# Optimization experiments

Measured on AMD Instinct MI355X. Metric: run time of the kernel, lower is better.

The kernel has to match this reference:

```python
import jax, jax.numpy as jnp
import numpy as np

K = 16  # top-k, matches init kwarg k


def _topk_weighted_mean(conn, parent, k):
    """conn: [n, p] weights, parent: [p, d] -> [n, d].
    Faithful to original: argsort()[-k:] top-k, softmax over selected weights,
    then weighted sum of gathered parent rows."""
    idx = jnp.argsort(conn, axis=-1)[:, -k:]                      # [n, k]
    w = jax.nn.softmax(jnp.take_along_axis(conn, idx, axis=-1), axis=-1)  # [n, k]
    return jnp.einsum('nk,nkd->nd', w, parent[idx])               # gather + small matmul


def setup_inputs() -> dict:
    key = jax.random.key(0)
    k_ids, k_c1, k_c2, k_c3, k_root = jax.random.split(key, 5)
    objNum, clusterNums, embedDim = 200000, (1024, 256, 64), 64
    batch = 8192
    return {
        'ids': jax.random.randint(k_ids, (batch,), 0, objNum, dtype=jnp.int64)
               if jax.config.jax_enable_x64 else jax.random.randint(k_ids, (batch,), 0, objNum, dtype=jnp.int32),
        'conn1': jax.random.normal(k_c1, (objNum, clusterNums[0]), jnp.float32),
        'conn2': jax.random.normal(k_c2, (clusterNums[0], clusterNums[1]), jnp.float32),
        'conn3': jax.random.normal(k_c3, (clusterNums[1], clusterNums[2]), jnp.float32),
        'rootMatrix': jax.random.normal(k_root, (clusterNums[2], embedDim), jnp.float32),
    }


def reference(ids, conn1, conn2, conn3, rootMatrix):
    # getEmbedByLevel(2): combine rootMatrix rows -> level-2 cluster embeddings
    e2 = _topk_weighted_mean(conn3, rootMatrix, K)   # [256, d]
    # getEmbedByLevel(1): combine level-2 embeddings -> level-1 cluster embeddings
    e1 = _topk_weighted_mean(conn2, e2, K)           # [1024, d]
    # getEmbed(ids): combine level-1 embeddings per requested leaf object
    return _topk_weighted_mean(conn1[ids], e1, K)    # [B, d]
```

## Files before the change

kernel.cpp:

```cpp
#include <hip/hip_runtime.h>
#include <stdint.h>
#include <math.h>

#define WAVE 64
#define TOPK 16

__device__ __forceinline__ uint32_t f2s(float f) {
    uint32_t u = __float_as_uint(f);
    return u ^ (uint32_t)(((int32_t)u >> 31) | 0x80000000);
}
__device__ __forceinline__ float s2f(uint32_t s) {
    uint32_t u = (s & 0x80000000u) ? (s ^ 0x80000000u) : ~s;
    return __uint_as_float(u);
}
__device__ __forceinline__ uint32_t umax32(uint32_t a, uint32_t b) { return a > b ? a : b; }

__device__ __forceinline__ uint32_t wave_max64(uint32_t m, int xaddr) {
    uint32_t r;
    r = (uint32_t)__builtin_amdgcn_update_dpp((int)m, (int)m, 0x121, 0xF, 0xF, false);
    m = umax32(m, r);
    r = (uint32_t)__builtin_amdgcn_update_dpp((int)m, (int)m, 0x122, 0xF, 0xF, false);
    m = umax32(m, r);
    r = (uint32_t)__builtin_amdgcn_update_dpp((int)m, (int)m, 0x124, 0xF, 0xF, false);
    m = umax32(m, r);
    r = (uint32_t)__builtin_amdgcn_update_dpp((int)m, (int)m, 0x128, 0xF, 0xF, false);
    m = umax32(m, r);
    r = (uint32_t)__builtin_amdgcn_ds_swizzle((int)m, 0x401F);
    m = umax32(m, r);
    r = (uint32_t)__builtin_amdgcn_ds_bpermute(xaddr, (int)m);
    m = umax32(m, r);
    return m;
}

template <int P>
__global__ void topk_wm_kernel(const float* __restrict__ conn,
                               const int* __restrict__ rowsel,
                               const float* __restrict__ parent,
                               float* __restrict__ out,
                               int n) {
    const int lane = threadIdx.x & (WAVE - 1);
    const int row = blockIdx.x * (blockDim.x >> 6) + (threadIdx.x >> 6);
    if (row >= n) return;

    const long src_row = rowsel ? (long)rowsel[row] : (long)row;
    const float* __restrict__ crow = conn + src_row * (long)P;

    constexpr int VPL = P / WAVE;
    uint32_t v[VPL];

    if constexpr (VPL >= 4) {
#pragma unroll
        for (int c = 0; c < VPL / 4; ++c) {
            float4 f4 = *reinterpret_cast<const float4*>(crow + c * (WAVE * 4) + lane * 4);
            v[c * 4 + 0] = f2s(f4.x);
            v[c * 4 + 1] = f2s(f4.y);
            v[c * 4 + 2] = f2s(f4.z);
            v[c * 4 + 3] = f2s(f4.w);
        }
    } else {
        v[0] = f2s(crow[lane]);
    }

    const int xaddr = (lane ^ 32) << 2;

    uint32_t topv[TOPK];
    int topi[TOPK];

#pragma unroll
    for (int t = 0; t < TOPK; ++t) {
        uint32_t m = v[0];
        int li = 0;
#pragma unroll
        for (int j = 1; j < VPL; ++j) {
            bool c = v[j] > m;
            m = c ? v[j] : m;
            li = c ? j : li;
        }
        const uint32_t m0 = m;
        m = wave_max64(m, xaddr);

        unsigned long long ball = __ballot(m0 == m);
        const int srcl = 63 - __builtin_clzll(ball);
        const int lis = __builtin_amdgcn_readlane(li, srcl);

        topv[t] = m;
        if constexpr (VPL >= 4) {
            topi[t] = (lis >> 2) * (WAVE * 4) + srcl * 4 + (lis & 3);
        } else {
            topi[t] = srcl;
        }

        const bool won = (lane == srcl);
#pragma unroll
        for (int j = 0; j < VPL; ++j) {
            if (won && j == lis) v[j] = 0u;
        }
    }

    const float mx = s2f(topv[0]);
    float w[TOPK];
    float ssum = 0.f;
#pragma unroll
    for (int t = 0; t < TOPK; ++t) {
        w[t] = __expf(s2f(topv[t]) - mx);
        ssum += w[t];
    }
    const float inv = 1.0f / ssum;

    float acc = 0.f;
#pragma unroll
    for (int t = 0; t < TOPK; ++t) {
        acc = fmaf(w[t], parent[topi[t] * 64 + lane], acc);
    }
    out[(long)row * 64 + lane] = acc * inv;
}

extern "C" void kernel_launch(void* const* d_in, const int* in_sizes, int n_in,
                              void* d_out, int out_size, void* d_ws, size_t ws_size,
                              hipStream_t stream) {
    const int* ids = (const int*)d_in[0];
    const float* conn1 = (const float*)d_in[1];
    const float* conn2 = (const float*)d_in[2];
    const float* conn3 = (const float*)d_in[3];
    const float* root = (const float*)d_in[4];
    float* out = (float*)d_out;

    const int batch = in_sizes[0];
    const int n1 = 1024, n2 = 256;

    float* e2 = (float*)d_ws;
    float* e1 = e2 + (size_t)n2 * 64;

    dim3 blk(256);

    topk_wm_kernel<64><<<dim3(n2 / 4), blk, 0, stream>>>(conn3, nullptr, root, e2, n2);
    topk_wm_kernel<256><<<dim3(n1 / 4), blk, 0, stream>>>(conn2, nullptr, e2, e1, n1);
    topk_wm_kernel<1024><<<dim3(batch / 4), blk, 0, stream>>>(conn1, ids, e1, out, batch);
}
```

Measured before the change: 36.30 us.

## Pack index into low key bits and pre-sort per-lane values for top-k selection

Each per-lane value is turned into a sortable key with its column index packed into the low bits, and the lane's values are bitonic-sorted in registers. Each top-k step then needs only a wave max of the lane head plus a register shift, with no ballot or readlane of the source lane. The wave reduction uses row_bcast DPP followed by readlane 63 instead of swizzle and bpermute. When the 16th and 17th keys tie in their truncated high bits, the kernel falls back to a full-precision selection pass, and the softmax reloads the exact selected values from memory. This adds in-register sort work per lane and a rarely-taken fallback branch.

```diff
diff --git a/kernel.cpp b/kernel.cpp
--- a/kernel.cpp
+++ b/kernel.cpp
@@ -7,29 +7,31 @@
 
 __device__ __forceinline__ uint32_t f2s(float f) {
     uint32_t u = __float_as_uint(f);
-    return u ^ (uint32_t)(((int32_t)u >> 31) | 0x80000000);
-}
-__device__ __forceinline__ float s2f(uint32_t s) {
-    uint32_t u = (s & 0x80000000u) ? (s ^ 0x80000000u) : ~s;
-    return __uint_as_float(u);
+    return u ^ (uint32_t)(((int32_t)u >> 31) | 0x80000000u);
 }
 __device__ __forceinline__ uint32_t umax32(uint32_t a, uint32_t b) { return a > b ? a : b; }
+__device__ __forceinline__ uint32_t umin32(uint32_t a, uint32_t b) { return a < b ? a : b; }
 
-__device__ __forceinline__ uint32_t wave_max64(uint32_t m, int xaddr) {
-    uint32_t r;
-    r = (uint32_t)__builtin_amdgcn_update_dpp((int)m, (int)m, 0x121, 0xF, 0xF, false);
-    m = umax32(m, r);
-    r = (uint32_t)__builtin_amdgcn_update_dpp((int)m, (int)m, 0x122, 0xF, 0xF, false);
-    m = umax32(m, r);
-    r = (uint32_t)__builtin_amdgcn_update_dpp((int)m, (int)m, 0x124, 0xF, 0xF, false);
-    m = umax32(m, r);
-    r = (uint32_t)__builtin_amdgcn_update_dpp((int)m, (int)m, 0x128, 0xF, 0xF, false);
-    m = umax32(m, r);
-    r = (uint32_t)__builtin_amdgcn_ds_swizzle((int)m, 0x401F);
-    m = umax32(m, r);
-    r = (uint32_t)__builtin_amdgcn_ds_bpermute(xaddr, (int)m);
-    m = umax32(m, r);
-    return m;
+template <int CTRL, int RMASK>
+__device__ __forceinline__ uint32_t dppmax(uint32_t m) {
+    uint32_t r = (uint32_t)__builtin_amdgcn_update_dpp((int)m, (int)m, CTRL, RMASK, 0xF, false);
+    return umax32(m, r);
+}
+
+__device__ __forceinline__ uint32_t wave_umax(uint32_t m) {
+    m = dppmax<0x121, 0xF>(m);
+    m = dppmax<0x122, 0xF>(m);
+    m = dppmax<0x124, 0xF>(m);
+    m = dppmax<0x128, 0xF>(m);
+    m = dppmax<0x142, 0xA>(m);
+    m = dppmax<0x143, 0xC>(m);
+    return (uint32_t)__builtin_amdgcn_readlane((int)m, 63);
+}
+
+template <int VPL>
+__device__ __forceinline__ uint32_t gpos(int j, int lane) {
+    if constexpr (VPL == 1) return (uint32_t)lane;
+    else return (uint32_t)((j >> 2) * (WAVE * 4) + lane * 4 + (j & 3));
 }
 
 template <int P>
@@ -38,6 +40,8 @@
                                const float* __restrict__ parent,
                                float* __restrict__ out,
                                int n) {
+    constexpr int VPL = P / WAVE;
+    constexpr uint32_t IMASK = (uint32_t)(P - 1);
     const int lane = threadIdx.x & (WAVE - 1);
     const int row = blockIdx.x * (blockDim.x >> 6) + (threadIdx.x >> 6);
     if (row >= n) return;
@@ -45,74 +49,107 @@
     const long src_row = rowsel ? (long)rowsel[row] : (long)row;
     const float* __restrict__ crow = conn + src_row * (long)P;
 
-    constexpr int VPL = P / WAVE;
-    uint32_t v[VPL];
-
-    if constexpr (VPL >= 4) {
+    uint32_t k[VPL];
+    if constexpr (VPL == 1) {
+        k[0] = (f2s(crow[lane]) & ~IMASK) | (uint32_t)lane;
+    } else {
 #pragma unroll
         for (int c = 0; c < VPL / 4; ++c) {
             float4 f4 = *reinterpret_cast<const float4*>(crow + c * (WAVE * 4) + lane * 4);
-            v[c * 4 + 0] = f2s(f4.x);
-            v[c * 4 + 1] = f2s(f4.y);
-            v[c * 4 + 2] = f2s(f4.z);
-            v[c * 4 + 3] = f2s(f4.w);
+            const uint32_t b = (uint32_t)(c * (WAVE * 4) + lane * 4);
+            k[c * 4 + 0] = (f2s(f4.x) & ~IMASK) | (b + 0u);
+            k[c * 4 + 1] = (f2s(f4.y) & ~IMASK) | (b + 1u);
+            k[c * 4 + 2] = (f2s(f4.z) & ~IMASK) | (b + 2u);
+            k[c * 4 + 3] = (f2s(f4.w) & ~IMASK) | (b + 3u);
         }
-    } else {
-        v[0] = f2s(crow[lane]);
-    }
-
-    const int xaddr = (lane ^ 32) << 2;
-
-    uint32_t topv[TOPK];
-    int topi[TOPK];
-
 #pragma unroll
-    for (int t = 0; t < TOPK; ++t) {
-        uint32_t m = v[0];
-        int li = 0;
+        for (int size = 2; size <= VPL; size <<= 1) {
 #pragma unroll
-        for (int j = 1; j < VPL; ++j) {
-            bool c = v[j] > m;
-            m = c ? v[j] : m;
-            li = c ? j : li;
-        }
-        const uint32_t m0 = m;
-        m = wave_max64(m, xaddr);
-
-        unsigned long long ball = __ballot(m0 == m);
-        const int srcl = 63 - __builtin_clzll(ball);
-        const int lis = __builtin_amdgcn_readlane(li, srcl);
-
-        topv[t] = m;
-        if constexpr (VPL >= 4) {
-            topi[t] = (lis >> 2) * (WAVE * 4) + srcl * 4 + (lis & 3);
-        } else {
-            topi[t] = srcl;
-        }
-
-        const bool won = (lane == srcl);
+            for (int stride = size >> 1; stride > 0; stride >>= 1) {
 #pragma unroll
-        for (int j = 0; j < VPL; ++j) {
-            if (won && j == lis) v[j] = 0u;
+                for (int i = 0; i < VPL; ++i) {
+                    const int j = i ^ stride;
+                    if (j > i) {
+                        const uint32_t a = k[i], b2 = k[j];
+                        const uint32_t hi = umax32(a, b2), lo = umin32(a, b2);
+                        if ((i & size) == 0) { k[i] = hi; k[j] = lo; }
+                        else                 { k[i] = lo; k[j] = hi; }
+                    }
+                }
+            }
         }
     }
 
-    const float mx = s2f(topv[0]);
-    float w[TOPK];
-    float ssum = 0.f;
+    uint32_t idx[TOPK];
+    uint32_t q16 = 0;
 #pragma unroll
     for (int t = 0; t < TOPK; ++t) {
-        w[t] = __expf(s2f(topv[t]) - mx);
-        ssum += w[t];
+        const uint32_t K = wave_umax(k[0]);
+        idx[t] = K & IMASK;
+        if (t == TOPK - 1) q16 = K & ~IMASK;
+        const bool won = (k[0] == K);
+#pragma unroll
+        for (int j = 0; j < VPL - 1; ++j) k[j] = won ? k[j + 1] : k[j];
+        k[VPL - 1] = won ? 0u : k[VPL - 1];
     }
-    const float inv = 1.0f / ssum;
+    const uint32_t k17 = wave_umax(k[0]);
 
-    float acc = 0.f;
+    if ((k17 & ~IMASK) == q16) {
+        uint32_t v[VPL];
+        if constexpr (VPL == 1) {
+            v[0] = f2s(crow[lane]);
+        } else {
+#pragma unroll
+            for (int c = 0; c < VPL / 4; ++c) {
+                float4 f4 = *reinterpret_cast<const float4*>(crow + c * (WAVE * 4) + lane * 4);
+                v[c * 4 + 0] = f2s(f4.x);
+                v[c * 4 + 1] = f2s(f4.y);
+                v[c * 4 + 2] = f2s(f4.z);
+                v[c * 4 + 3] = f2s(f4.w);
+            }
+        }
+#pragma unroll
+        for (int t = 0; t < TOPK; ++t) {
+            uint32_t m = v[0];
+            int li = 0;
+#pragma unroll
+            for (int j = 1; j < VPL; ++j) {
+                bool c = v[j] >= m;
+                m = c ? v[j] : m;
+                li = c ? j : li;
+            }
+            uint32_t gi = gpos<VPL>(li, lane);
+            const uint32_t mygi = gi;
+            uint32_t mm = m;
+#pragma unroll
+            for (int off = 32; off > 0; off >>= 1) {
+                uint32_t om = (uint32_t)__shfl_xor((int)mm, off);
+                uint32_t og = (uint32_t)__shfl_xor((int)gi, off);
+                bool c = (om > mm) || (om == mm && og > gi);
+                mm = c ? om : mm;
+                gi = c ? og : gi;
+            }
+            idx[t] = gi;
+            const bool won = (mygi == gi) && (m == mm);
+#pragma unroll
+            for (int j = 0; j < VPL; ++j) {
+                if (won && j == li) v[j] = 0u;
+            }
+        }
+    }
+
+    float vsel[TOPK];
+#pragma unroll
+    for (int t = 0; t < TOPK; ++t) vsel[t] = crow[idx[t]];
+    const float v0 = vsel[0];
+    float ssum = 0.f, acc = 0.f;
 #pragma unroll
     for (int t = 0; t < TOPK; ++t) {
-        acc = fmaf(w[t], parent[topi[t] * 64 + lane], acc);
+        const float w = __expf(vsel[t] - v0);
+        ssum += w;
+        acc = fmaf(w, parent[idx[t] * 64u + (uint32_t)lane], acc);
     }
-    out[(long)row * 64 + lane] = acc * inv;
+    out[(long)row * 64 + lane] = acc / ssum;
 }
 
 extern "C" void kernel_launch(void* const* d_in, const int* in_sizes, int n_in,
```

Result: faster. 33.92 us (-6.6%).
